# Performance work log

Measured on AMD Instinct MI355X. Metric: run time of the kernel, lower is better.

Reference implementation:

```python
import jax, jax.numpy as jnp
import numpy as np

N = 1_000_000   # total points
C = 20          # semantic classes
B = 4           # scenes in batch
L = 200         # instance label vocabulary
INST = 64       # number of proposals/instances
M = 300_000     # masked points (len(object_idxs))
T = 320_000     # total proposal rows
IGNORE = -100
PREPARE_EPOCHS = 128


def setup_inputs() -> dict:
    key = jax.random.key(0)
    ks = jax.random.split(key, 12)
    semantic_scores = jax.random.normal(ks[0], (N, C), jnp.float32)
    semantic_labels = jax.random.randint(ks[1], (N,), 0, C)
    lab = jax.random.randint(ks[2], (N,), 0, L)
    ign = jax.random.uniform(ks[3], (N,)) < 0.05
    instance_labels = jnp.where(ign, IGNORE, lab)
    pt_offsets = jax.random.normal(ks[4], (N, 3), jnp.float32)
    instance_info = jax.random.normal(ks[5], (N, 9), jnp.float32)
    coords = jax.random.normal(ks[6], (N, 3), jnp.float32)
    mask_logits = jax.random.normal(ks[7], (INST, M), jnp.float32)
    object_idxs = jax.random.randint(ks[8], (M,), 0, N)
    col1 = jax.random.randint(ks[9], (T,), 0, N)
    proposals_idx_shift = jnp.stack([jnp.zeros_like(col1), col1], axis=1)
    mids = jnp.sort(jax.random.randint(ks[10], (INST - 1,), 0, T))
    proposals_offset_shift = jnp.concatenate(
        [jnp.zeros((1,), jnp.int32), mids.astype(jnp.int32), jnp.full((1,), T, jnp.int32)])
    inst_batch_ids = jax.random.randint(ks[11], (INST,), 0, B)
    batch_offsets = jnp.array([0, N // 4, N // 2, 3 * N // 4, N], dtype=jnp.int32)
    batch_ids = jnp.clip(jnp.searchsorted(batch_offsets, object_idxs, side='right') - 1, 0, B - 1)
    inst_pred_seg_label = jax.random.randint(jax.random.fold_in(key, 99), (INST,), 0, C)
    return dict(semantic_scores=semantic_scores, pt_offsets=pt_offsets,
                instance_info=instance_info, coords=coords, mask_logits=mask_logits,
                semantic_labels=semantic_labels, instance_labels=instance_labels,
                object_idxs=object_idxs, proposals_idx_shift=proposals_idx_shift,
                proposals_offset_shift=proposals_offset_shift, inst_batch_ids=inst_batch_ids,
                batch_ids=batch_ids, batch_offsets=batch_offsets,
                inst_pred_seg_label=inst_pred_seg_label, epoch=200)


def reference(semantic_scores, pt_offsets, instance_info, coords, mask_logits,
              semantic_labels, instance_labels, object_idxs, proposals_idx_shift,
              proposals_offset_shift, inst_batch_ids, batch_ids, batch_offsets,
              inst_pred_seg_label, epoch):
    f32 = jnp.float32
    n_pts = semantic_scores.shape[0]
    n_inst, m_pts = mask_logits.shape
    n_batch = batch_offsets.shape[0] - 1
    LW = L + 1  # label buckets, bucket 0 == ignore(-100)

    # --- semantic cross entropy (ignore_index) ---
    logp = jax.nn.log_softmax(semantic_scores, axis=-1)
    sem_valid = semantic_labels != IGNORE
    safe_lab = jnp.where(sem_valid, semantic_labels, 0)
    nll = -jnp.take_along_axis(logp, safe_lab[:, None], axis=1)[:, 0]
    semantic_loss = jnp.sum(nll * sem_valid) / jnp.maximum(jnp.sum(sem_valid), 1)

    # --- offset losses ---
    gt_offsets = instance_info[:, 0:3] - coords
    pt_dist = jnp.sum(jnp.abs(pt_offsets - gt_offsets), axis=-1)
    valid = (instance_labels != IGNORE).astype(f32)
    vsum = jnp.sum(valid) + 1e-6
    offset_norm_loss = jnp.sum(pt_dist * valid) / vsum
    gt_u = gt_offsets / (jnp.linalg.norm(gt_offsets, axis=1, keepdims=True) + 1e-8)
    pt_u = pt_offsets / (jnp.linalg.norm(pt_offsets, axis=1, keepdims=True) + 1e-8)
    offset_dir_loss = jnp.sum(-jnp.sum(gt_u * pt_u, axis=-1) * valid) / vsum

    loss = semantic_loss + offset_norm_loss + offset_dir_loss

    if epoch > PREPARE_EPOCHS:
        # map instance labels to ids: ignore -> 0, label l -> l+1 (order-preserving, so
        # argmax-first tie-break == torch.mode smallest-value tie-break)
        labels_id = jnp.where(instance_labels == IGNORE, 0, instance_labels + 1)
        # segment id per proposal row from CSR offsets
        seg = jnp.clip(jnp.searchsorted(proposals_offset_shift, jnp.arange(T), side='right') - 1,
                       0, n_inst - 1)
        prop_lab = labels_id[proposals_idx_shift[:, 1]]
        hist = jax.ops.segment_sum(jnp.ones((T,), f32), seg * LW + prop_lab,
                                   num_segments=n_inst * LW).reshape(n_inst, LW)
        mode_id = jnp.argmax(hist, axis=1)                       # [INST] per-instance mode vote

        masked_lab = labels_id[object_idxs]                      # [M]
        sem_masked = semantic_labels[object_idxs]                # [M]
        skip = (mode_id == 0) | (inst_pred_seg_label <= 3)       # [INST]

        batch_match = inst_batch_ids[:, None] == batch_ids[None, :]           # [INST,M]
        sem_match = inst_pred_seg_label[:, None] == sem_masked[None, :]       # [INST,M]
        weights = batch_match.astype(f32) * jnp.where(skip[:, None], 1.0,
                                                      sem_match.astype(f32))  # [INST,M]

        # per-batch label histograms (full points and masked points)
        point_batch = jnp.clip(jnp.searchsorted(batch_offsets, jnp.arange(n_pts),
                                                side='right') - 1, 0, n_batch - 1)
        hist_full = jax.ops.segment_sum(jnp.ones((n_pts,), f32), point_batch * LW + labels_id,
                                        num_segments=n_batch * LW).reshape(n_batch, LW)
        hist_mask = jax.ops.segment_sum(jnp.ones((m_pts,), f32), batch_ids * LW + masked_lab,
                                        num_segments=n_batch * LW).reshape(n_batch, LW)
        num = hist_mask[inst_batch_ids, mode_id]
        den = hist_full[inst_batch_ids, mode_id]
        cover = jnp.where(den > 0, num / den, 0.0)
        pos = (~skip) & (cover > 0.3)
        inst_gt_mask = (pos[:, None] & (masked_lab[None, :] == mode_id[:, None])).astype(f32)

        pred = jax.nn.sigmoid(mask_logits)
        wb = (weights > 0).astype(f32)
        inter = jnp.sum(wb * pred * inst_gt_mask, axis=1)
        union = jnp.sum(wb * pred * pred, axis=1) + jnp.sum(wb * inst_gt_mask * inst_gt_mask, axis=1) + 1e-5
        dice_n = 1.0 - 2.0 * inter / union
        dice_valid = (~skip) & (jnp.sum(wb, axis=1) > 0)
        dice_loss = jnp.sum(jnp.where(dice_valid, dice_n, 0.0)) / (jnp.sum(dice_valid.astype(f32)) + 1e-6)

        # BCE(sigmoid(x), t) in stable form: softplus(x) - t*x
        bce = jax.nn.softplus(mask_logits) - inst_gt_mask * mask_logits
        score_loss = jnp.sum(bce * weights) / (jnp.sum(weights) + 1e-6)

        loss = loss + score_loss + dice_loss
    return loss
```

## Files before the change

kernel.cpp:

```cpp
#include <hip/hip_runtime.h>
#include <math.h>

namespace {

constexpr int N_PTS  = 1000000;
constexpr int C_CLS  = 20;
constexpr int N_B    = 4;
constexpr int L_LAB  = 200;
constexpr int LW     = L_LAB + 1;
constexpr int N_INST = 64;
constexpr int M_PTS  = 300000;
constexpr int T_PROP = 320000;
constexpr int IGN    = -100;
constexpr int PREP   = 128;

constexpr size_t OFF_G      = 0;
constexpr size_t OFF_INTER  = 64;
constexpr size_t OFF_UP     = 576;
constexpr size_t OFF_UG     = 1088;
constexpr size_t OFF_WBS    = 1600;
constexpr size_t OFF_SN     = 2112;
constexpr size_t OFF_HFULL  = 2624;
constexpr size_t OFF_HMASK  = 5840;
constexpr size_t OFF_IHIST  = 9056;
constexpr size_t OFF_FLAGS  = 60512;
constexpr size_t ZERO_BYTES = 60768;
constexpr size_t OFF_META   = 60800;
constexpr size_t WS_REQUIRED = OFF_META + (size_t)M_PTS * 2;

__device__ __forceinline__ float waveSumF(float v) {
  #pragma unroll
  for (int off = 32; off > 0; off >>= 1) v += __shfl_down(v, off, 64);
  return v;
}
__device__ __forceinline__ int waveMaxI(int v) {
  #pragma unroll
  for (int off = 32; off > 0; off >>= 1) v = max(v, __shfl_down(v, off, 64));
  return v;
}

constexpr int PB_PT   = 1024;
constexpr int PB_HF   = 256;
constexpr int PB_PROP = 256;
constexpr int PB_HM   = 256;
constexpr int A_BLOCKS = PB_PT + PB_HF + PB_PROP + PB_HM;

__global__ __launch_bounds__(256) void k_A(const float* __restrict__ scores,
                                           const float* __restrict__ pt_off,
                                           const float* __restrict__ info,
                                           const float* __restrict__ coords,
                                           const int* __restrict__ sem_lab,
                                           const int* __restrict__ inst_lab,
                                           const int* __restrict__ obj_idx,
                                           const int* __restrict__ batch_ids,
                                           const int* __restrict__ prop_idx,
                                           const int* __restrict__ prop_off,
                                           const int* __restrict__ batch_off,
                                           double* __restrict__ g,
                                           int* __restrict__ hist_full,
                                           int* __restrict__ hist_mask,
                                           int* __restrict__ inst_hist,
                                           unsigned short* __restrict__ meta,
                                           int write_meta) {
  __shared__ int sh[N_B * LW];
  const int bx = blockIdx.x;

  if (bx < PB_PT) {
    float s_nll = 0.f, s_cnt = 0.f, s_dist = 0.f, s_dir = 0.f, s_val = 0.f;
    const int gid = bx * blockDim.x + threadIdx.x;
    const int p0  = gid * 4;
    if (p0 < N_PTS) {
      const int4 sl4 = *reinterpret_cast<const int4*>(sem_lab + p0);
      const int4 il4 = *reinterpret_cast<const int4*>(inst_lab + p0);
      const float4* c4 = reinterpret_cast<const float4*>(coords + (size_t)p0 * 3);
      const float4 ca = c4[0], cb = c4[1], cc = c4[2];
      const float4* o4 = reinterpret_cast<const float4*>(pt_off + (size_t)p0 * 3);
      const float4 oa = o4[0], ob = o4[1], oc = o4[2];
      const float4* i4 = reinterpret_cast<const float4*>(info + (size_t)p0 * 9);
      const float4 f0 = i4[0], f2 = i4[2], f4 = i4[4], f5 = i4[5], f6 = i4[6], f7 = i4[7];
      const float cx[4] = { ca.x, ca.w, cb.z, cc.y };
      const float cy[4] = { ca.y, cb.x, cb.w, cc.z };
      const float cz[4] = { ca.z, cb.y, cc.x, cc.w };
      const float ox[4] = { oa.x, oa.w, ob.z, oc.y };
      const float oy[4] = { oa.y, ob.x, ob.w, oc.z };
      const float oz[4] = { oa.z, ob.y, oc.x, oc.w };
      const float ix[4] = { f0.x, f2.y, f4.z, f6.w };
      const float iy[4] = { f0.y, f2.z, f4.w, f7.x };
      const float iz[4] = { f0.z, f2.w, f5.x, f7.y };
      const int sl[4] = { sl4.x, sl4.y, sl4.z, sl4.w };
      const int il[4] = { il4.x, il4.y, il4.z, il4.w };
      #pragma unroll
      for (int k = 0; k < 4; ++k) {
        const int p = p0 + k;
        const float4* r4 = reinterpret_cast<const float4*>(scores + (size_t)p * C_CLS);
        float x[C_CLS];
        #pragma unroll
        for (int q = 0; q < C_CLS / 4; ++q) {
          const float4 v = r4[q];
          x[4 * q + 0] = v.x; x[4 * q + 1] = v.y; x[4 * q + 2] = v.z; x[4 * q + 3] = v.w;
        }
        float mx = x[0];
        #pragma unroll
        for (int c = 1; c < C_CLS; ++c) mx = fmaxf(mx, x[c]);
        float se = 0.f;
        #pragma unroll
        for (int c = 0; c < C_CLS; ++c) se += __expf(x[c] - mx);
        const float lse = mx + __logf(se);
        if (sl[k] != IGN) { s_nll += lse - x[sl[k]]; s_cnt += 1.f; }
        const float gx = ix[k] - cx[k];
        const float gy = iy[k] - cy[k];
        const float gz = iz[k] - cz[k];
        if (il[k] != IGN) {
          s_val  += 1.f;
          s_dist += fabsf(ox[k] - gx) + fabsf(oy[k] - gy) + fabsf(oz[k] - gz);
          const float gn = sqrtf(gx * gx + gy * gy + gz * gz) + 1e-8f;
          const float pn = sqrtf(ox[k] * ox[k] + oy[k] * oy[k] + oz[k] * oz[k]) + 1e-8f;
          s_dir += -((gx * ox[k] + gy * oy[k] + gz * oz[k]) / (gn * pn));
        }
      }
    }
    float* red = reinterpret_cast<float*>(sh);
    float vals[5] = { s_nll, s_cnt, s_dist, s_dir, s_val };
    const int lane = threadIdx.x & 63, wv = threadIdx.x >> 6;
    #pragma unroll
    for (int k = 0; k < 5; ++k) {
      const float t = waveSumF(vals[k]);
      if (lane == 0) red[k * 4 + wv] = t;
    }
    __syncthreads();
    if (threadIdx.x < 5) {
      const float s = red[threadIdx.x * 4 + 0] + red[threadIdx.x * 4 + 1] +
                      red[threadIdx.x * 4 + 2] + red[threadIdx.x * 4 + 3];
      atomicAdd(&g[threadIdx.x], (double)s);
    }
  } else if (bx < PB_PT + PB_HF) {
    for (int t = threadIdx.x; t < N_B * LW; t += blockDim.x) sh[t] = 0;
    __syncthreads();
    const int b1 = batch_off[1], b2 = batch_off[2], b3 = batch_off[3];
    const int blk = bx - PB_PT;
    const int4* il4p = reinterpret_cast<const int4*>(inst_lab);
    const int nq = N_PTS / 4;
    for (int q = blk * blockDim.x + threadIdx.x; q < nq; q += PB_HF * blockDim.x) {
      const int4 v = il4p[q];
      const int p = q * 4;
      const int ils[4] = { v.x, v.y, v.z, v.w };
      #pragma unroll
      for (int k = 0; k < 4; ++k) {
        const int lab = (ils[k] == IGN) ? 0 : (ils[k] + 1);
        const int pp = p + k;
        int pb = 0;
        if (pp >= b1) pb = 1;
        if (pp >= b2) pb = 2;
        if (pp >= b3) pb = 3;
        atomicAdd(&sh[pb * LW + lab], 1);
      }
    }
    __syncthreads();
    for (int t = threadIdx.x; t < N_B * LW; t += blockDim.x)
      if (sh[t]) atomicAdd(&hist_full[t], sh[t]);
  } else if (bx < PB_PT + PB_HF + PB_PROP) {
    if (threadIdx.x <= N_INST) sh[threadIdx.x] = prop_off[threadIdx.x];
    __syncthreads();
    const int blk = bx - PB_PT - PB_HF;
    const int4* pi4 = reinterpret_cast<const int4*>(prop_idx);
    const int nq = T_PROP / 2;
    for (int q = blk * blockDim.x + threadIdx.x; q < nq; q += PB_PROP * blockDim.x) {
      const int4 v = pi4[q];
      const int t0 = 2 * q, t1 = 2 * q + 1;
      const int il0 = inst_lab[v.y];
      const int il1 = inst_lab[v.w];
      int lo0 = 0, hi0 = N_INST + 1, lo1 = 0, hi1 = N_INST + 1;
      #pragma unroll
      for (int s = 0; s < 7; ++s) {
        const int m0 = (lo0 + hi0) >> 1;
        if (m0 <= N_INST && sh[m0] <= t0) lo0 = m0 + 1; else hi0 = m0;
        const int m1 = (lo1 + hi1) >> 1;
        if (m1 <= N_INST && sh[m1] <= t1) lo1 = m1 + 1; else hi1 = m1;
      }
      const int seg0 = min(lo0 - 1, N_INST - 1);
      const int seg1 = min(lo1 - 1, N_INST - 1);
      const int lab0 = (il0 == IGN) ? 0 : (il0 + 1);
      const int lab1 = (il1 == IGN) ? 0 : (il1 + 1);
      atomicAdd(&inst_hist[seg0 * LW + lab0], 1);
      atomicAdd(&inst_hist[seg1 * LW + lab1], 1);
    }
  } else {
    for (int t = threadIdx.x; t < N_B * LW; t += blockDim.x) sh[t] = 0;
    __syncthreads();
    const int blk = bx - PB_PT - PB_HF - PB_PROP;
    const int4* oi4 = reinterpret_cast<const int4*>(obj_idx);
    const int4* bi4 = reinterpret_cast<const int4*>(batch_ids);
    ushort4* m4 = reinterpret_cast<ushort4*>(meta);
    const int nq = M_PTS / 4;
    for (int q = blk * blockDim.x + threadIdx.x; q < nq; q += PB_HM * blockDim.x) {
      const int4 o = oi4[q];
      const int4 b = bi4[q];
      const int il0 = inst_lab[o.x], il1 = inst_lab[o.y],
                il2 = inst_lab[o.z], il3 = inst_lab[o.w];
      const int sm0 = sem_lab[o.x], sm1 = sem_lab[o.y],
                sm2 = sem_lab[o.z], sm3 = sem_lab[o.w];
      const int ml0 = (il0 == IGN) ? 0 : (il0 + 1);
      const int ml1 = (il1 == IGN) ? 0 : (il1 + 1);
      const int ml2 = (il2 == IGN) ? 0 : (il2 + 1);
      const int ml3 = (il3 == IGN) ? 0 : (il3 + 1);
      atomicAdd(&sh[b.x * LW + ml0], 1);
      atomicAdd(&sh[b.y * LW + ml1], 1);
      atomicAdd(&sh[b.z * LW + ml2], 1);
      atomicAdd(&sh[b.w * LW + ml3], 1);
      if (write_meta) {
        ushort4 mm;
        mm.x = (unsigned short)(ml0 | (sm0 << 8) | (b.x << 13));
        mm.y = (unsigned short)(ml1 | (sm1 << 8) | (b.y << 13));
        mm.z = (unsigned short)(ml2 | (sm2 << 8) | (b.z << 13));
        mm.w = (unsigned short)(ml3 | (sm3 << 8) | (b.w << 13));
        m4[q] = mm;
      }
    }
    __syncthreads();
    for (int t = threadIdx.x; t < N_B * LW; t += blockDim.x)
      if (sh[t]) atomicAdd(&hist_mask[t], sh[t]);
  }
}

__global__ __launch_bounds__(256) void k_argmax(const int* __restrict__ inst_hist,
                                                const int* __restrict__ hist_full,
                                                const int* __restrict__ hist_mask,
                                                const int* __restrict__ inst_batch_ids,
                                                const int* __restrict__ inst_seg,
                                                int* __restrict__ flags) {
  __shared__ int red[4];
  const int i = blockIdx.x;
  const int t = threadIdx.x;
  int key = 0;
  if (t < LW) {
    const int cnt = inst_hist[i * LW + t];
    key = (cnt << 8) | (255 - t);
  }
  key = waveMaxI(key);
  const int lane = t & 63, wv = t >> 6;
  if (lane == 0) red[wv] = key;
  __syncthreads();
  if (t == 0) {
    int k = max(max(red[0], red[1]), max(red[2], red[3]));
    const int m = 255 - (k & 0xFF);
    const int b = inst_batch_ids[i];
    const int seg = inst_seg[i];
    const bool skip = (m == 0) || (seg <= 3);
    const float num = (float)hist_mask[b * LW + m];
    const float den = (float)hist_full[b * LW + m];
    const float cover = (den > 0.f) ? (num / den) : 0.f;
    const bool pos = (!skip) && (cover > 0.3f);
    flags[i] = m | (skip ? 0x100 : 0) | (pos ? 0x200 : 0) | (b << 10) | (seg << 12);
  }
}

template <bool USE_META>
__global__ __launch_bounds__(256) void k_mask(const float* __restrict__ logits,
                                              const unsigned short* __restrict__ meta,
                                              const int* __restrict__ obj_idx,
                                              const int* __restrict__ inst_lab,
                                              const int* __restrict__ sem_lab,
                                              const int* __restrict__ batch_ids,
                                              const int* __restrict__ flags,
                                              double* __restrict__ i_inter,
                                              double* __restrict__ i_up,
                                              double* __restrict__ i_ug,
                                              double* __restrict__ i_wbs,
                                              double* __restrict__ i_sn) {
  const int i  = blockIdx.y;
  const int fl = flags[i];
  const int  mode_i = fl & 0xFF;
  const bool skip   = (fl >> 8) & 1;
  const bool pos    = (fl >> 9) & 1;
  const int  bi     = (fl >> 10) & 3;
  const int  seg    = (fl >> 12) & 31;

  float inter = 0.f, up = 0.f, ug = 0.f, wbs = 0.f, sn = 0.f;

  if (USE_META) {
    const float4* row4 = reinterpret_cast<const float4*>(logits + (size_t)i * M_PTS);
    const ushort4* m4  = reinterpret_cast<const ushort4*>(meta);
    const int nq = M_PTS / 4;
    for (int q = blockIdx.x * blockDim.x + threadIdx.x; q < nq; q += gridDim.x * blockDim.x) {
      const float4  x4 = row4[q];
      const ushort4 d4 = m4[q];
      const float xs[4] = { x4.x, x4.y, x4.z, x4.w };
      const int   ds[4] = { d4.x, d4.y, d4.z, d4.w };
      #pragma unroll
      for (int k = 0; k < 4; ++k) {
        const int md = ds[k];
        const int ml = md & 0xFF;
        const int sm = (md >> 8) & 31;
        const int b  = (md >> 13) & 3;
        const bool w  = (b == bi) && (skip || (sm == seg));
        const bool gt = pos && (ml == mode_i);
        const float x  = xs[k];
        const float e  = __expf(-fabsf(x));
        const float r  = __builtin_amdgcn_rcpf(1.f + e);
        const float pr = (x >= 0.f) ? r : e * r;
        const float sp = fmaxf(x, 0.f) + __logf(1.f + e);
        const float wf = w ? 1.f : 0.f;
        const float gf = gt ? 1.f : 0.f;
        up    += wf * pr * pr;
        wbs   += wf;
        sn    += wf * (sp - gf * x);
        inter += wf * gf * pr;
        ug    += wf * gf;
      }
    }
  } else {
    const float* row = logits + (size_t)i * M_PTS;
    for (int j = blockIdx.x * blockDim.x + threadIdx.x; j < M_PTS; j += gridDim.x * blockDim.x) {
      const int o  = obj_idx[j];
      const int il = inst_lab[o];
      const int ml = (il == IGN) ? 0 : (il + 1);
      const int sm = sem_lab[o];
      const int b  = batch_ids[j];
      const bool w  = (b == bi) && (skip || (sm == seg));
      const bool gt = pos && (ml == mode_i);
      const float x  = row[j];
      const float e  = __expf(-fabsf(x));
      const float r  = __builtin_amdgcn_rcpf(1.f + e);
      const float pr = (x >= 0.f) ? r : e * r;
      const float sp = fmaxf(x, 0.f) + __logf(1.f + e);
      const float wf = w ? 1.f : 0.f;
      const float gf = gt ? 1.f : 0.f;
      up    += wf * pr * pr;
      wbs   += wf;
      sn    += wf * (sp - gf * x);
      inter += wf * gf * pr;
      ug    += wf * gf;
    }
  }

  __shared__ float red[5][4];
  float vals[5] = { inter, up, ug, wbs, sn };
  const int lane = threadIdx.x & 63, wv = threadIdx.x >> 6;
  #pragma unroll
  for (int k = 0; k < 5; ++k) {
    const float t = waveSumF(vals[k]);
    if (lane == 0) red[k][wv] = t;
  }
  __syncthreads();
  if (threadIdx.x < 5) {
    const float s = red[threadIdx.x][0] + red[threadIdx.x][1] + red[threadIdx.x][2] + red[threadIdx.x][3];
    double* dst = (threadIdx.x == 0) ? (i_inter + i)
                : (threadIdx.x == 1) ? (i_up + i)
                : (threadIdx.x == 2) ? (i_ug + i)
                : (threadIdx.x == 3) ? (i_wbs + i)
                                     : (i_sn + i);
    atomicAdd(dst, (double)s);
  }
}

__global__ void k_final(const double* __restrict__ g,
                        const double* __restrict__ i_inter,
                        const double* __restrict__ i_up,
                        const double* __restrict__ i_ug,
                        const double* __restrict__ i_wbs,
                        const double* __restrict__ i_sn,
                        const int* __restrict__ flags,
                        const int* __restrict__ epoch,
                        float* __restrict__ out) {
  if (threadIdx.x != 0 || blockIdx.x != 0) return;
  double loss = g[0] / fmax(g[1], 1.0);
  const double vsum = g[4] + 1e-6;
  loss += g[2] / vsum + g[3] / vsum;
  if (epoch[0] > PREP) {
    double sn = 0.0, wsum = 0.0, dice = 0.0, dcnt = 0.0;
    for (int i = 0; i < N_INST; ++i) {
      wsum += i_wbs[i];
      sn   += i_sn[i];
      const bool skip = (flags[i] >> 8) & 1;
      if (!skip && i_wbs[i] > 0.0) {
        const double un = i_up[i] + i_ug[i] + 1e-5;
        dice += 1.0 - 2.0 * i_inter[i] / un;
        dcnt += 1.0;
      }
    }
    loss += sn / (wsum + 1e-6) + dice / (dcnt + 1e-6);
  }
  out[0] = (float)loss;
}

}

extern "C" void kernel_launch(void* const* d_in, const int* in_sizes, int n_in,
                              void* d_out, int out_size, void* d_ws, size_t ws_size,
                              hipStream_t stream) {
  const float* semantic_scores  = (const float*)d_in[0];
  const float* pt_offsets       = (const float*)d_in[1];
  const float* instance_info    = (const float*)d_in[2];
  const float* coords           = (const float*)d_in[3];
  const float* mask_logits      = (const float*)d_in[4];
  const int*   semantic_labels  = (const int*)d_in[5];
  const int*   instance_labels  = (const int*)d_in[6];
  const int*   object_idxs      = (const int*)d_in[7];
  const int*   proposals_idx    = (const int*)d_in[8];
  const int*   proposals_off    = (const int*)d_in[9];
  const int*   inst_batch_ids   = (const int*)d_in[10];
  const int*   batch_ids        = (const int*)d_in[11];
  const int*   batch_offsets    = (const int*)d_in[12];
  const int*   inst_seg         = (const int*)d_in[13];
  const int*   epoch            = (const int*)d_in[14];
  float* out = (float*)d_out;

  char* w = (char*)d_ws;
  double* g        = (double*)(w + OFF_G);
  double* i_inter  = (double*)(w + OFF_INTER);
  double* i_up     = (double*)(w + OFF_UP);
  double* i_ug     = (double*)(w + OFF_UG);
  double* i_wbs    = (double*)(w + OFF_WBS);
  double* i_sn     = (double*)(w + OFF_SN);
  int* hist_full   = (int*)(w + OFF_HFULL);
  int* hist_mask   = (int*)(w + OFF_HMASK);
  int* inst_hist   = (int*)(w + OFF_IHIST);
  int* flags       = (int*)(w + OFF_FLAGS);
  unsigned short* meta = (unsigned short*)(w + OFF_META);

  const bool use_meta = (ws_size >= WS_REQUIRED);

  (void)hipMemsetAsync(d_ws, 0, ZERO_BYTES, stream);

  k_A<<<A_BLOCKS, 256, 0, stream>>>(semantic_scores, pt_offsets, instance_info, coords,
                                    semantic_labels, instance_labels, object_idxs,
                                    batch_ids, proposals_idx, proposals_off, batch_offsets,
                                    g, hist_full, hist_mask, inst_hist, meta,
                                    use_meta ? 1 : 0);

  k_argmax<<<N_INST, 256, 0, stream>>>(inst_hist, hist_full, hist_mask,
                                       inst_batch_ids, inst_seg, flags);

  dim3 mgrid(40, N_INST);
  if (use_meta) {
    k_mask<true><<<mgrid, 256, 0, stream>>>(mask_logits, meta, object_idxs, instance_labels,
                                            semantic_labels, batch_ids, flags,
                                            i_inter, i_up, i_ug, i_wbs, i_sn);
  } else {
    k_mask<false><<<mgrid, 256, 0, stream>>>(mask_logits, meta, object_idxs, instance_labels,
                                             semantic_labels, batch_ids, flags,
                                             i_inter, i_up, i_ug, i_wbs, i_sn);
  }
  k_final<<<1, 64, 0, stream>>>(g, i_inter, i_up, i_ug, i_wbs, i_sn, flags, epoch, out);
}
```

Before: 297.0 us.

## Stage point tiles through LDS, fold argmax into mask kernel, unroll mask loop

The per-point loss blocks now load scores, coords, offsets and instance info with coalesced float4 reads into shared memory, one point per thread in tiles of 256. Before, each thread issued strided per-point vector loads. The separate argmax kernel is removed, and each mask block recomputes the instance's mode label and flags itself, which saves one launch but repeats the work in every block. The mask kernel grid is halved and each thread processes two float4 chunks per iteration to raise memory-level parallelism. Points 1 and 2 of this description add LDS use and extra syncs, which may lower occupancy of k_A.

```diff
diff --git a/kernel.cpp b/kernel.cpp
--- a/kernel.cpp
+++ b/kernel.cpp
@@ -39,11 +39,18 @@
   return v;
 }
 
-constexpr int PB_PT   = 1024;
 constexpr int PB_HF   = 256;
 constexpr int PB_PROP = 256;
 constexpr int PB_HM   = 256;
-constexpr int A_BLOCKS = PB_PT + PB_HF + PB_PROP + PB_HM;
+constexpr int PB_PRE  = PB_HF + PB_PROP + PB_HM;
+constexpr int PT_TILES = (N_PTS + 255) / 256;
+constexpr int A_BLOCKS = PB_PRE + PT_TILES;
+
+constexpr int LDS_SC = 256 * 21;
+constexpr int LDS_CO = LDS_SC;
+constexpr int LDS_OF = LDS_CO + 768;
+constexpr int LDS_IN = LDS_OF + 768;
+constexpr int LDS_FLOATS = LDS_IN + 768;
 
 __global__ __launch_bounds__(256) void k_A(const float* __restrict__ scores,
                                            const float* __restrict__ pt_off,
@@ -62,85 +69,18 @@
                                            int* __restrict__ inst_hist,
                                            unsigned short* __restrict__ meta,
                                            int write_meta) {
-  __shared__ int sh[N_B * LW];
+  __shared__ float s_f[LDS_FLOATS];
+  int* sh = reinterpret_cast<int*>(s_f);
   const int bx = blockIdx.x;
-
-  if (bx < PB_PT) {
-    float s_nll = 0.f, s_cnt = 0.f, s_dist = 0.f, s_dir = 0.f, s_val = 0.f;
-    const int gid = bx * blockDim.x + threadIdx.x;
-    const int p0  = gid * 4;
-    if (p0 < N_PTS) {
-      const int4 sl4 = *reinterpret_cast<const int4*>(sem_lab + p0);
-      const int4 il4 = *reinterpret_cast<const int4*>(inst_lab + p0);
-      const float4* c4 = reinterpret_cast<const float4*>(coords + (size_t)p0 * 3);
-      const float4 ca = c4[0], cb = c4[1], cc = c4[2];
-      const float4* o4 = reinterpret_cast<const float4*>(pt_off + (size_t)p0 * 3);
-      const float4 oa = o4[0], ob = o4[1], oc = o4[2];
-      const float4* i4 = reinterpret_cast<const float4*>(info + (size_t)p0 * 9);
-      const float4 f0 = i4[0], f2 = i4[2], f4 = i4[4], f5 = i4[5], f6 = i4[6], f7 = i4[7];
-      const float cx[4] = { ca.x, ca.w, cb.z, cc.y };
-      const float cy[4] = { ca.y, cb.x, cb.w, cc.z };
-      const float cz[4] = { ca.z, cb.y, cc.x, cc.w };
-      const float ox[4] = { oa.x, oa.w, ob.z, oc.y };
-      const float oy[4] = { oa.y, ob.x, ob.w, oc.z };
-      const float oz[4] = { oa.z, ob.y, oc.x, oc.w };
-      const float ix[4] = { f0.x, f2.y, f4.z, f6.w };
-      const float iy[4] = { f0.y, f2.z, f4.w, f7.x };
-      const float iz[4] = { f0.z, f2.w, f5.x, f7.y };
-      const int sl[4] = { sl4.x, sl4.y, sl4.z, sl4.w };
-      const int il[4] = { il4.x, il4.y, il4.z, il4.w };
-      #pragma unroll
-      for (int k = 0; k < 4; ++k) {
-        const int p = p0 + k;
-        const float4* r4 = reinterpret_cast<const float4*>(scores + (size_t)p * C_CLS);
-        float x[C_CLS];
-        #pragma unroll
-        for (int q = 0; q < C_CLS / 4; ++q) {
-          const float4 v = r4[q];
-          x[4 * q + 0] = v.x; x[4 * q + 1] = v.y; x[4 * q + 2] = v.z; x[4 * q + 3] = v.w;
-        }
-        float mx = x[0];
-        #pragma unroll
-        for (int c = 1; c < C_CLS; ++c) mx = fmaxf(mx, x[c]);
-        float se = 0.f;
-        #pragma unroll
-        for (int c = 0; c < C_CLS; ++c) se += __expf(x[c] - mx);
-        const float lse = mx + __logf(se);
-        if (sl[k] != IGN) { s_nll += lse - x[sl[k]]; s_cnt += 1.f; }
-        const float gx = ix[k] - cx[k];
-        const float gy = iy[k] - cy[k];
-        const float gz = iz[k] - cz[k];
-        if (il[k] != IGN) {
-          s_val  += 1.f;
-          s_dist += fabsf(ox[k] - gx) + fabsf(oy[k] - gy) + fabsf(oz[k] - gz);
-          const float gn = sqrtf(gx * gx + gy * gy + gz * gz) + 1e-8f;
-          const float pn = sqrtf(ox[k] * ox[k] + oy[k] * oy[k] + oz[k] * oz[k]) + 1e-8f;
-          s_dir += -((gx * ox[k] + gy * oy[k] + gz * oz[k]) / (gn * pn));
-        }
-      }
-    }
-    float* red = reinterpret_cast<float*>(sh);
-    float vals[5] = { s_nll, s_cnt, s_dist, s_dir, s_val };
-    const int lane = threadIdx.x & 63, wv = threadIdx.x >> 6;
-    #pragma unroll
-    for (int k = 0; k < 5; ++k) {
-      const float t = waveSumF(vals[k]);
-      if (lane == 0) red[k * 4 + wv] = t;
-    }
-    __syncthreads();
-    if (threadIdx.x < 5) {
-      const float s = red[threadIdx.x * 4 + 0] + red[threadIdx.x * 4 + 1] +
-                      red[threadIdx.x * 4 + 2] + red[threadIdx.x * 4 + 3];
-      atomicAdd(&g[threadIdx.x], (double)s);
-    }
-  } else if (bx < PB_PT + PB_HF) {
-    for (int t = threadIdx.x; t < N_B * LW; t += blockDim.x) sh[t] = 0;
+  const int t  = threadIdx.x;
+
+  if (bx < PB_HF) {
+    for (int k = t; k < N_B * LW; k += blockDim.x) sh[k] = 0;
     __syncthreads();
     const int b1 = batch_off[1], b2 = batch_off[2], b3 = batch_off[3];
-    const int blk = bx - PB_PT;
     const int4* il4p = reinterpret_cast<const int4*>(inst_lab);
     const int nq = N_PTS / 4;
-    for (int q = blk * blockDim.x + threadIdx.x; q < nq; q += PB_HF * blockDim.x) {
+    for (int q = bx * blockDim.x + t; q < nq; q += PB_HF * blockDim.x) {
       const int4 v = il4p[q];
       const int p = q * 4;
       const int ils[4] = { v.x, v.y, v.z, v.w };
@@ -156,15 +96,15 @@
       }
     }
     __syncthreads();
-    for (int t = threadIdx.x; t < N_B * LW; t += blockDim.x)
-      if (sh[t]) atomicAdd(&hist_full[t], sh[t]);
-  } else if (bx < PB_PT + PB_HF + PB_PROP) {
-    if (threadIdx.x <= N_INST) sh[threadIdx.x] = prop_off[threadIdx.x];
-    __syncthreads();
-    const int blk = bx - PB_PT - PB_HF;
+    for (int k = t; k < N_B * LW; k += blockDim.x)
+      if (sh[k]) atomicAdd(&hist_full[k], sh[k]);
+  } else if (bx < PB_HF + PB_PROP) {
+    if (t <= N_INST) sh[t] = prop_off[t];
+    __syncthreads();
+    const int blk = bx - PB_HF;
     const int4* pi4 = reinterpret_cast<const int4*>(prop_idx);
     const int nq = T_PROP / 2;
-    for (int q = blk * blockDim.x + threadIdx.x; q < nq; q += PB_PROP * blockDim.x) {
+    for (int q = blk * blockDim.x + t; q < nq; q += PB_PROP * blockDim.x) {
       const int4 v = pi4[q];
       const int t0 = 2 * q, t1 = 2 * q + 1;
       const int il0 = inst_lab[v.y];
@@ -184,15 +124,15 @@
       atomicAdd(&inst_hist[seg0 * LW + lab0], 1);
       atomicAdd(&inst_hist[seg1 * LW + lab1], 1);
     }
-  } else {
-    for (int t = threadIdx.x; t < N_B * LW; t += blockDim.x) sh[t] = 0;
-    __syncthreads();
-    const int blk = bx - PB_PT - PB_HF - PB_PROP;
+  } else if (bx < PB_PRE) {
+    for (int k = t; k < N_B * LW; k += blockDim.x) sh[k] = 0;
+    __syncthreads();
+    const int blk = bx - PB_HF - PB_PROP;
     const int4* oi4 = reinterpret_cast<const int4*>(obj_idx);
     const int4* bi4 = reinterpret_cast<const int4*>(batch_ids);
     ushort4* m4 = reinterpret_cast<ushort4*>(meta);
     const int nq = M_PTS / 4;
-    for (int q = blk * blockDim.x + threadIdx.x; q < nq; q += PB_HM * blockDim.x) {
+    for (int q = blk * blockDim.x + t; q < nq; q += PB_HM * blockDim.x) {
       const int4 o = oi4[q];
       const int4 b = bi4[q];
       const int il0 = inst_lab[o.x], il1 = inst_lab[o.y],
@@ -217,40 +157,109 @@
       }
     }
     __syncthreads();
-    for (int t = threadIdx.x; t < N_B * LW; t += blockDim.x)
-      if (sh[t]) atomicAdd(&hist_mask[t], sh[t]);
-  }
-}
-
-__global__ __launch_bounds__(256) void k_argmax(const int* __restrict__ inst_hist,
-                                                const int* __restrict__ hist_full,
-                                                const int* __restrict__ hist_mask,
-                                                const int* __restrict__ inst_batch_ids,
-                                                const int* __restrict__ inst_seg,
-                                                int* __restrict__ flags) {
-  __shared__ int red[4];
-  const int i = blockIdx.x;
-  const int t = threadIdx.x;
-  int key = 0;
-  if (t < LW) {
-    const int cnt = inst_hist[i * LW + t];
-    key = (cnt << 8) | (255 - t);
-  }
-  key = waveMaxI(key);
-  const int lane = t & 63, wv = t >> 6;
-  if (lane == 0) red[wv] = key;
-  __syncthreads();
-  if (t == 0) {
-    int k = max(max(red[0], red[1]), max(red[2], red[3]));
-    const int m = 255 - (k & 0xFF);
-    const int b = inst_batch_ids[i];
-    const int seg = inst_seg[i];
-    const bool skip = (m == 0) || (seg <= 3);
-    const float num = (float)hist_mask[b * LW + m];
-    const float den = (float)hist_full[b * LW + m];
-    const float cover = (den > 0.f) ? (num / den) : 0.f;
-    const bool pos = (!skip) && (cover > 0.3f);
-    flags[i] = m | (skip ? 0x100 : 0) | (pos ? 0x200 : 0) | (b << 10) | (seg << 12);
+    for (int k = t; k < N_B * LW; k += blockDim.x)
+      if (sh[k]) atomicAdd(&hist_mask[k], sh[k]);
+  } else {
+    const int P0 = (bx - PB_PRE) * 256;
+    {
+      const float4* sc4 = reinterpret_cast<const float4*>(scores);
+      const int base = P0 * 5;
+      #pragma unroll
+      for (int k = 0; k < 5; ++k) {
+        const int fr = k * 256 + t;
+        const int f  = base + fr;
+        if (f < N_PTS * 5) {
+          const float4 v = sc4[f];
+          const int p_rel = fr / 5, c4 = fr % 5;
+          float* dst = &s_f[p_rel * 21 + c4 * 4];
+          dst[0] = v.x; dst[1] = v.y; dst[2] = v.z; dst[3] = v.w;
+        }
+      }
+    }
+    if (t < 192) {
+      const float4* c4p = reinterpret_cast<const float4*>(coords);
+      const float4* o4p = reinterpret_cast<const float4*>(pt_off);
+      const int f = P0 * 3 / 4 + t;
+      if (f < N_PTS * 3 / 4) {
+        const float4 cv = c4p[f];
+        const float4 ov = o4p[f];
+        float* dc = &s_f[LDS_CO + 4 * t];
+        float* dо = &s_f[LDS_OF + 4 * t];
+        dc[0] = cv.x; dc[1] = cv.y; dc[2] = cv.z; dc[3] = cv.w;
+        dо[0] = ov.x; dо[1] = ov.y; dо[2] = ov.z; dо[3] = ov.w;
+      }
+    }
+    {
+      const float4* i4p = reinterpret_cast<const float4*>(info);
+      const int base = P0 * 9 / 4;
+      #pragma unroll
+      for (int k = 0; k < 3; ++k) {
+        const int fr = k * 256 + t;
+        if (fr < 576) {
+          const int f = base + fr;
+          if (f < N_PTS * 9 / 4) {
+            const float4 v = i4p[f];
+            const float vs[4] = { v.x, v.y, v.z, v.w };
+            const int l = 4 * fr;
+            #pragma unroll
+            for (int i = 0; i < 4; ++i) {
+              const int li = l + i;
+              const int p_rel = li / 9, c = li % 9;
+              if (c < 3) s_f[LDS_IN + p_rel * 3 + c] = vs[i];
+            }
+          }
+        }
+      }
+    }
+    __syncthreads();
+
+    float s_nll = 0.f, s_cnt = 0.f, s_dist = 0.f, s_dir = 0.f, s_val = 0.f;
+    const int p = P0 + t;
+    if (p < N_PTS) {
+      const int sl = sem_lab[p];
+      const int il = inst_lab[p];
+      float x[C_CLS];
+      #pragma unroll
+      for (int c = 0; c < C_CLS; ++c) x[c] = s_f[t * 21 + c];
+      float mx = x[0];
+      #pragma unroll
+      for (int c = 1; c < C_CLS; ++c) mx = fmaxf(mx, x[c]);
+      float se = 0.f;
+      #pragma unroll
+      for (int c = 0; c < C_CLS; ++c) se += __expf(x[c] - mx);
+      const float lse = mx + __logf(se);
+      if (sl != IGN) { s_nll = lse - x[sl]; s_cnt = 1.f; }
+      const float cx = s_f[LDS_CO + 3 * t + 0];
+      const float cy = s_f[LDS_CO + 3 * t + 1];
+      const float cz = s_f[LDS_CO + 3 * t + 2];
+      const float ox = s_f[LDS_OF + 3 * t + 0];
+      const float oy = s_f[LDS_OF + 3 * t + 1];
+      const float oz = s_f[LDS_OF + 3 * t + 2];
+      const float gx = s_f[LDS_IN + 3 * t + 0] - cx;
+      const float gy = s_f[LDS_IN + 3 * t + 1] - cy;
+      const float gz = s_f[LDS_IN + 3 * t + 2] - cz;
+      if (il != IGN) {
+        s_val  = 1.f;
+        s_dist = fabsf(ox - gx) + fabsf(oy - gy) + fabsf(oz - gz);
+        const float gn = sqrtf(gx * gx + gy * gy + gz * gz) + 1e-8f;
+        const float pn = sqrtf(ox * ox + oy * oy + oz * oz) + 1e-8f;
+        s_dir = -((gx * ox + gy * oy + gz * oz) / (gn * pn));
+      }
+    }
+    __syncthreads();
+    float* red = s_f;
+    float vals[5] = { s_nll, s_cnt, s_dist, s_dir, s_val };
+    const int lane = t & 63, wv = t >> 6;
+    #pragma unroll
+    for (int k = 0; k < 5; ++k) {
+      const float r = waveSumF(vals[k]);
+      if (lane == 0) red[k * 4 + wv] = r;
+    }
+    __syncthreads();
+    if (t < 5) {
+      const float s = red[t * 4 + 0] + red[t * 4 + 1] + red[t * 4 + 2] + red[t * 4 + 3];
+      atomicAdd(&g[t], (double)s);
+    }
   }
 }
 
@@ -261,14 +270,45 @@
                                               const int* __restrict__ inst_lab,
                                               const int* __restrict__ sem_lab,
                                               const int* __restrict__ batch_ids,
-                                              const int* __restrict__ flags,
+                                              const int* __restrict__ inst_hist,
+                                              const int* __restrict__ hist_full,
+                                              const int* __restrict__ hist_mask,
+                                              const int* __restrict__ inst_batch_ids,
+                                              const int* __restrict__ inst_seg,
+                                              int* __restrict__ flags,
                                               double* __restrict__ i_inter,
                                               double* __restrict__ i_up,
                                               double* __restrict__ i_ug,
                                               double* __restrict__ i_wbs,
                                               double* __restrict__ i_sn) {
-  const int i  = blockIdx.y;
-  const int fl = flags[i];
+  const int i = blockIdx.y;
+  const int t = threadIdx.x;
+  __shared__ int skey[4];
+  __shared__ int sflag;
+  {
+    int key = 0;
+    if (t < LW) key = (inst_hist[i * LW + t] << 8) | (255 - t);
+    key = waveMaxI(key);
+    const int lane = t & 63, wv = t >> 6;
+    if (lane == 0) skey[wv] = key;
+    __syncthreads();
+    if (t == 0) {
+      const int k = max(max(skey[0], skey[1]), max(skey[2], skey[3]));
+      const int m = 255 - (k & 0xFF);
+      const int b = inst_batch_ids[i];
+      const int seg = inst_seg[i];
+      const bool skip = (m == 0) || (seg <= 3);
+      const float num = (float)hist_mask[b * LW + m];
+      const float den = (float)hist_full[b * LW + m];
+      const float cover = (den > 0.f) ? (num / den) : 0.f;
+      const bool pos = (!skip) && (cover > 0.3f);
+      const int fl = m | (skip ? 0x100 : 0) | (pos ? 0x200 : 0) | (b << 10) | (seg << 12);
+      sflag = fl;
+      if (blockIdx.x == 0) flags[i] = fl;
+    }
+    __syncthreads();
+  }
+  const int fl = sflag;
   const int  mode_i = fl & 0xFF;
   const bool skip   = (fl >> 8) & 1;
   const bool pos    = (fl >> 9) & 1;
@@ -281,13 +321,20 @@
     const float4* row4 = reinterpret_cast<const float4*>(logits + (size_t)i * M_PTS);
     const ushort4* m4  = reinterpret_cast<const ushort4*>(meta);
     const int nq = M_PTS / 4;
-    for (int q = blockIdx.x * blockDim.x + threadIdx.x; q < nq; q += gridDim.x * blockDim.x) {
-      const float4  x4 = row4[q];
-      const ushort4 d4 = m4[q];
-      const float xs[4] = { x4.x, x4.y, x4.z, x4.w };
-      const int   ds[4] = { d4.x, d4.y, d4.z, d4.w };
-      #pragma unroll
-      for (int k = 0; k < 4; ++k) {
+    const int step = gridDim.x * blockDim.x;
+    for (int q = blockIdx.x * blockDim.x + t; q < nq; q += 2 * step) {
+      const int q2 = q + step;
+      const bool has2 = q2 < nq;
+      const float4  xa = row4[q];
+      const ushort4 da = m4[q];
+      float4  xb = xa; ushort4 db = da;
+      if (has2) { xb = row4[q2]; db = m4[q2]; }
+      const float xs[8] = { xa.x, xa.y, xa.z, xa.w, xb.x, xb.y, xb.z, xb.w };
+      const int   ds[8] = { da.x, da.y, da.z, da.w, db.x, db.y, db.z, db.w };
+      const int nk = has2 ? 8 : 4;
+      #pragma unroll
+      for (int k = 0; k < 8; ++k) {
+        if (k >= nk) break;
         const int md = ds[k];
         const int ml = md & 0xFF;
         const int sm = (md >> 8) & 31;
@@ -310,7 +357,7 @@
     }
   } else {
     const float* row = logits + (size_t)i * M_PTS;
-    for (int j = blockIdx.x * blockDim.x + threadIdx.x; j < M_PTS; j += gridDim.x * blockDim.x) {
+    for (int j = blockIdx.x * blockDim.x + t; j < M_PTS; j += gridDim.x * blockDim.x) {
       const int o  = obj_idx[j];
       const int il = inst_lab[o];
       const int ml = (il == IGN) ? 0 : (il + 1);
@@ -335,20 +382,20 @@
 
   __shared__ float red[5][4];
   float vals[5] = { inter, up, ug, wbs, sn };
-  const int lane = threadIdx.x & 63, wv = threadIdx.x >> 6;
+  const int lane = t & 63, wv = t >> 6;
   #pragma unroll
   for (int k = 0; k < 5; ++k) {
-    const float t = waveSumF(vals[k]);
-    if (lane == 0) red[k][wv] = t;
+    const float r = waveSumF(vals[k]);
+    if (lane == 0) red[k][wv] = r;
   }
   __syncthreads();
-  if (threadIdx.x < 5) {
-    const float s = red[threadIdx.x][0] + red[threadIdx.x][1] + red[threadIdx.x][2] + red[threadIdx.x][3];
-    double* dst = (threadIdx.x == 0) ? (i_inter + i)
-                : (threadIdx.x == 1) ? (i_up + i)
-                : (threadIdx.x == 2) ? (i_ug + i)
-                : (threadIdx.x == 3) ? (i_wbs + i)
-                                     : (i_sn + i);
+  if (t < 5) {
+    const float s = red[t][0] + red[t][1] + red[t][2] + red[t][3];
+    double* dst = (t == 0) ? (i_inter + i)
+                : (t == 1) ? (i_up + i)
+                : (t == 2) ? (i_ug + i)
+                : (t == 3) ? (i_wbs + i)
+                           : (i_sn + i);
     atomicAdd(dst, (double)s);
   }
 }
@@ -428,18 +475,17 @@
                                     g, hist_full, hist_mask, inst_hist, meta,
                                     use_meta ? 1 : 0);
 
-  k_argmax<<<N_INST, 256, 0, stream>>>(inst_hist, hist_full, hist_mask,
-                                       inst_batch_ids, inst_seg, flags);
-
-  dim3 mgrid(40, N_INST);
+  dim3 mgrid(20, N_INST);
   if (use_meta) {
     k_mask<true><<<mgrid, 256, 0, stream>>>(mask_logits, meta, object_idxs, instance_labels,
-                                            semantic_labels, batch_ids, flags,
-                                            i_inter, i_up, i_ug, i_wbs, i_sn);
+                                            semantic_labels, batch_ids, inst_hist,
+                                            hist_full, hist_mask, inst_batch_ids, inst_seg,
+                                            flags, i_inter, i_up, i_ug, i_wbs, i_sn);
   } else {
     k_mask<false><<<mgrid, 256, 0, stream>>>(mask_logits, meta, object_idxs, instance_labels,
-                                             semantic_labels, batch_ids, flags,
-                                             i_inter, i_up, i_ug, i_wbs, i_sn);
+                                             semantic_labels, batch_ids, inst_hist,
+                                             hist_full, hist_mask, inst_batch_ids, inst_seg,
+                                             flags, i_inter, i_up, i_ug, i_wbs, i_sn);
   }
   k_final<<<1, 64, 0, stream>>>(g, i_inter, i_up, i_ug, i_wbs, i_sn, flags, epoch, out);
 }
```

Measured after the change: 300.8 us. Within noise of the previous version (+1.3%).
